# Kernel optimization log

Measured on AMD Instinct MI355X. Metric: run time of the kernel, lower is better.

The kernel has to match this reference:

```python
import jax, jax.numpy as jnp
from jax import lax
import numpy as np

# static config matching init_kwargs
PROPOSAL_COUNT = 1000
NMS_THRESH = 0.7
MIN_SIZE = 16.0
IMG_H, IMG_W = 512, 512
NUM_ANCHORS = 262144
BATCH = 16
PRE_NMS = min(6000, NUM_ANCHORS)


def setup_inputs() -> dict:
    key = jax.random.key(0)
    k1, k2, k3, k4, k5 = jax.random.split(key, 5)
    # realistic anchors: centers uniform in image, sizes in [16, 160]
    cx = jax.random.uniform(k1, (NUM_ANCHORS,), minval=0.0, maxval=float(IMG_W))
    cy = jax.random.uniform(k2, (NUM_ANCHORS,), minval=0.0, maxval=float(IMG_H))
    w = jax.random.uniform(k3, (NUM_ANCHORS,), minval=16.0, maxval=160.0)
    h = jax.random.uniform(k4, (NUM_ANCHORS,), minval=16.0, maxval=160.0)
    anchors = jnp.stack([cx - 0.5 * w, cy - 0.5 * h, cx + 0.5 * w, cy + 0.5 * h], axis=1)
    ka, kb = jax.random.split(k5)
    rpn_class_probs = jax.random.uniform(ka, (BATCH, NUM_ANCHORS, 2), dtype=jnp.float32)
    rpn_bbox_deltas = jax.random.normal(kb, (BATCH, NUM_ANCHORS, 4), dtype=jnp.float32) * 0.2
    return {"anchors": anchors, "rpn_class_probs": rpn_class_probs, "rpn_bbox_deltas": rpn_bbox_deltas}


def apply_box_deltas(anchors, deltas):
    # standard (dx, dy, dw, dh) decode in center form
    w = anchors[:, 2] - anchors[:, 0]
    h = anchors[:, 3] - anchors[:, 1]
    cx = anchors[:, 0] + 0.5 * w
    cy = anchors[:, 1] + 0.5 * h
    cx = cx + deltas[:, 0] * w
    cy = cy + deltas[:, 1] * h
    w = w * jnp.exp(deltas[:, 2])
    h = h * jnp.exp(deltas[:, 3])
    return jnp.stack([cx - 0.5 * w, cy - 0.5 * h, cx + 0.5 * w, cy + 0.5 * h], axis=1)


def nms_keep(boxes, valid):
    # greedy NMS over score-sorted boxes [n,4]; invalid boxes start suppressed
    x1, y1, x2, y2 = boxes[:, 0], boxes[:, 1], boxes[:, 2], boxes[:, 3]
    areas = (x2 - x1) * (y2 - y1)
    n = boxes.shape[0]

    def body(i, state):
        suppressed, keep = state
        is_valid = jnp.logical_not(suppressed[i])
        keep = keep.at[i].set(is_valid)
        xx1 = jnp.maximum(x1[i], x1)
        yy1 = jnp.maximum(y1[i], y1)
        xx2 = jnp.minimum(x2[i], x2)
        yy2 = jnp.minimum(y2[i], y2)
        inter = jnp.maximum(xx2 - xx1, 0.0) * jnp.maximum(yy2 - yy1, 0.0)
        iou = inter / (areas[i] + areas - inter + 1e-9)
        iou = iou.at[i].set(0.0)  # never self-suppress
        suppressed = suppressed | (is_valid & (iou > NMS_THRESH))
        return suppressed, keep

    suppressed0 = jnp.logical_not(valid)
    keep0 = jnp.zeros((n,), dtype=bool)
    _, keep = lax.fori_loop(0, n, body, (suppressed0, keep0))
    return keep


def _per_image(scores, deltas, anchors):
    boxes = apply_box_deltas(anchors, deltas)
    boxes = jnp.stack([
        jnp.clip(boxes[:, 0], 0.0, IMG_W - 1.0),
        jnp.clip(boxes[:, 1], 0.0, IMG_H - 1.0),
        jnp.clip(boxes[:, 2], 0.0, IMG_W - 1.0),
        jnp.clip(boxes[:, 3], 0.0, IMG_H - 1.0),
    ], axis=1)
    ws = boxes[:, 2] - boxes[:, 0]
    hs = boxes[:, 3] - boxes[:, 1]
    valid = (ws >= MIN_SIZE) & (hs >= MIN_SIZE)
    # emulate boolean filter + descending sort with fixed shapes:
    # invalid boxes get -inf score so they sort to the back and start suppressed.
    masked = jnp.where(valid, scores, -jnp.inf)
    order = jnp.argsort(-masked)[:PRE_NMS]
    boxes_s = boxes[order]
    valid_s = valid[order]
    keep = nms_keep(lax.stop_gradient(boxes_s), valid_s)
    idx = jnp.flatnonzero(keep, size=PROPOSAL_COUNT, fill_value=PRE_NMS)
    boxes_pad = jnp.concatenate([boxes_s, jnp.zeros((1, 4), boxes_s.dtype)], axis=0)
    return boxes_pad[idx]  # [proposal_count, 4], zero-padded like torch


def reference(anchors, rpn_class_probs, rpn_bbox_deltas):
    fg_scores = rpn_class_probs[:, :, 1]
    return jax.vmap(_per_image, in_axes=(0, 0, None))(fg_scores, rpn_bbox_deltas, anchors)
```

## Files before the change

kernel.cpp:

```cpp
#include <hip/hip_runtime.h>
#include <cstdint>

#define B 16
#define N 262144
#define PRE 6000
#define KOUT 1000
#define MW 94
#define CW 24
#define NTILE 300
#define ECAP 4096
#define RMAX 64
#define NBIN 2049
#define PREFILT 1967
#define PGATE 0.9599609375f
#define IMGMAX 511.0f
#define NMS_TH 0.7f

typedef unsigned int u32;
typedef unsigned long long u64;

#define OFF_MASK  0ull
#define OFF_SEL   72192000ull
#define OFF_BOX   74289152ull
#define OFF_VAL   75829248ull
#define OFF_HIST  75841536ull
#define OFF_CAB   75972864ull
#define OFF_BCNT  76104192ull
#define OFF_T     76235520ull
#define OFF_M     76235584ull
#define OFF_FLAG  76235648ull
#define OFF_ECNT  76235712ull
#define OFF_EDG   76235776ull
#define OFF_DW    76497920ull
#define OFF_PL    76825600ull
#define OFF_PCNT  78922752ull
#define WS_NEED   78922816ull

__device__ __forceinline__ void box_from(const float4 a, const float4 d,
    float& x1, float& y1, float& x2, float& y2, bool& valid) {
#pragma clang fp contract(off)
  float w  = a.z - a.x;
  float h  = a.w - a.y;
  float cx = a.x + 0.5f * w;
  float cy = a.y + 0.5f * h;
  cx = cx + d.x * w;
  cy = cy + d.y * h;
  w = w * expf(d.z);
  h = h * expf(d.w);
  x1 = cx - 0.5f * w;
  y1 = cy - 0.5f * h;
  x2 = cx + 0.5f * w;
  y2 = cy + 0.5f * h;
  x1 = fminf(fmaxf(x1, 0.0f), IMGMAX);
  y1 = fminf(fmaxf(y1, 0.0f), IMGMAX);
  x2 = fminf(fmaxf(x2, 0.0f), IMGMAX);
  y2 = fminf(fmaxf(y2, 0.0f), IMGMAX);
  valid = ((x2 - x1) >= 16.0f) && ((y2 - y1) >= 16.0f);
}

__device__ __forceinline__ bool iou_gt(float inter, float denom) {
  float d = inter - NMS_TH * denom;
  if (__builtin_expect(fabsf(d) <= 1e-4f * denom, 0))
    return (inter / denom) > NMS_TH;
  return d > 0.0f;
}

__device__ __forceinline__ int bin_of(u32 u) {
  if (u == 0u) return 0;
  float s = __uint_as_float(u & 0x7FFFFFFFu);
  return 1 + min(2047, (int)(s * 2048.0f));
}

__global__ void k_hist(const float4* __restrict__ anch, const float2* __restrict__ probs,
                       const float4* __restrict__ delt, u32* __restrict__ hist,
                       float4* __restrict__ boxes, u64* __restrict__ plist,
                       u32* __restrict__ pcnt) {
  __shared__ u32 sh[128];
  __shared__ u64 pbuf[256];
  __shared__ u32 pcl, pbase;
  int t = threadIdx.x;
  int img = blockIdx.y;
  if (t == 0) pcl = 0;
  if (blockIdx.x == 0 && t < 16)
    boxes[(size_t)img * 6016 + 6000 + t] = make_float4(0.f, 0.f, 0.f, 0.f);
  if (t < 128) sh[t] = 0;
  __syncthreads();
  const float4* pr4 = (const float4*)(probs + (size_t)img * N);
  int b4 = blockIdx.x * 1024 + t;
  float4 p0 = pr4[b4];
  float4 p1 = pr4[b4 + 256];
  float4 p2 = pr4[b4 + 512];
  float4 p3 = pr4[b4 + 768];
  auto handle = [&](float s, int i) {
    if (s >= PGATE) {
      float4 a = anch[i];
      float4 d = delt[(size_t)img * N + i];
      float x1, y1, x2, y2; bool valid;
      box_from(a, d, x1, y1, x2, y2, valid);
      if (valid) {
        int bin = 1 + min(2047, (int)(s * 2048.0f));
        atomicAdd(&sh[bin - 1921], 1u);
        u64 key = ((u64)(__float_as_uint(s) | 0x80000000u) << 32)
                | (u64)(0xFFFFFFFFu - (u32)i);
        u32 p = atomicAdd(&pcl, 1u);
        if (p < 256u) pbuf[p] = key;
      }
    }
  };
  handle(p0.y, 2 * b4);            handle(p0.w, 2 * b4 + 1);
  handle(p1.y, 2 * (b4 + 256));    handle(p1.w, 2 * (b4 + 256) + 1);
  handle(p2.y, 2 * (b4 + 512));    handle(p2.w, 2 * (b4 + 512) + 1);
  handle(p3.y, 2 * (b4 + 768));    handle(p3.w, 2 * (b4 + 768) + 1);
  __syncthreads();
  if (t < 128 && sh[t]) atomicAdd(&hist[img * 2052 + 1921 + t], sh[t]);
  u32 n = min(pcl, 256u);
  if (t == 0) {
    if (pcl > 256u) atomicAdd(&pcnt[img], 1000000u);
    pbase = n ? atomicAdd(&pcnt[img], n) : 0u;
  }
  __syncthreads();
  for (u32 p = t; p < n; p += 256) {
    u32 dp = pbase + p;
    if (dp < 16384u) plist[(size_t)img * 16384 + dp] = pbuf[p];
  }
}

__global__ void k_thresh(const u32* __restrict__ hist, int* __restrict__ Tarr,
                         u32* __restrict__ cab, u32* __restrict__ Marr) {
  int img = blockIdx.x;
  int l = threadIdx.x;
  const u32* hb = hist + img * 2052;
  u32 v0 = hb[1921 + 2 * l];
  u32 v1 = hb[1922 + 2 * l];
  u32 csum = v0 + v1;
  u32 sfx = csum;
  for (int off = 1; off < 64; off <<= 1) {
    u32 tv = __shfl_down(sfx, off);
    if (l + off < 64) sfx += tv;
  }
  u32 excl = sfx - csum;
  u32* cb = cab + img * 2052;
  cb[1921 + 2 * l] = excl + v1;
  cb[1922 + 2 * l] = excl;
  u32 sfxP = __shfl(excl, 22);
  bool ok = (sfxP >= (u32)PRE);
  if (l == 0 && !ok) { Tarr[img] = -1; Marr[img] = 0; }
  if (ok && excl < (u32)PRE && sfx >= (u32)PRE) {
    int T; u32 M;
    if (excl + v1 >= (u32)PRE) { T = 1922 + 2 * l; M = excl + v1; }
    else                       { T = 1921 + 2 * l; M = sfx; }
    Tarr[img] = T; Marr[img] = M;
  }
}

__global__ void k_hist_fb(const float4* __restrict__ anch, const float2* __restrict__ probs,
                          const float4* __restrict__ delt, const int* __restrict__ Tarr,
                          u32* __restrict__ hist) {
  int img = blockIdx.y;
  if (Tarr[img] >= 0) return;
  __shared__ u32 sh[NBIN];
  int t = threadIdx.x;
  for (int p = t; p < NBIN; p += 256) sh[p] = 0;
  __syncthreads();
  int base = blockIdx.x * 1024;
  for (int r = 0; r < 4; r++) {
    int i = base + r * 256 + t;
    float4 a = anch[i];
    float4 d = delt[(size_t)img * N + i];
    float s = probs[(size_t)img * N + i].y;
    float x1, y1, x2, y2; bool valid;
    box_from(a, d, x1, y1, x2, y2, valid);
    int bin = valid ? (1 + min(2047, (int)(s * 2048.0f))) : 0;
    if (bin < PREFILT) atomicAdd(&sh[bin], 1u);
  }
  __syncthreads();
  for (int p = t; p < NBIN; p += 256)
    if (sh[p]) atomicAdd(&hist[img * 2052 + p], sh[p]);
}

__global__ void k_thresh_fb(const u32* __restrict__ hist, int* __restrict__ Tarr,
                            u32* __restrict__ cab, u32* __restrict__ Marr) {
  int img = blockIdx.x;
  if (Tarr[img] >= 0) return;
  int l = threadIdx.x;
  const u32* hb = hist + img * 2052;
  u32 v[32];
  u32 csum = 0;
#pragma unroll
  for (int k = 0; k < 32; k++) { v[k] = hb[l * 32 + 1 + k]; csum += v[k]; }
  u32 sfx = csum;
  for (int off = 1; off < 64; off <<= 1) {
    u32 tv = __shfl_down(sfx, off);
    if (l + off < 64) sfx += tv;
  }
  u32 excl = sfx - csum;
  u32 ss = 0;
  u32 outv[32];
#pragma unroll
  for (int k = 31; k >= 0; k--) { outv[k] = ss + excl; ss += v[k]; }
  u32* cb = cab + img * 2052;
#pragma unroll
  for (int k = 0; k < 32; k++) cb[l * 32 + 1 + k] = outv[k];
  u32 total = __shfl(sfx, 0);
  if (l == 0) cb[0] = total;
  if (l == 0 && total < PRE) { Tarr[img] = 0; Marr[img] = 16384u; }
  if (excl < PRE && sfx >= PRE) {
    u32 acc = excl; int T = 0; u32 Mv = 0;
#pragma unroll
    for (int k = 31; k >= 0; k--) {
      acc += v[k];
      if (acc >= PRE) { T = l * 32 + 1 + k; Mv = acc; break; }
    }
    Tarr[img] = T; Marr[img] = Mv;
  }
}

__global__ void k_compact_fast(const u64* __restrict__ plist, const u32* __restrict__ pcnt,
                               const int* __restrict__ Tarr, const u32* __restrict__ cab,
                               u32* __restrict__ bincnt, u64* __restrict__ sel) {
  int t = threadIdx.x, img = blockIdx.y;
  int T = Tarr[img];
  u32 P = pcnt[img];
  if (T < PREFILT || P > 16384u) return;
  const u32* cb = cab + img * 2052;
  for (u32 i = blockIdx.x * 256u + (u32)t; i < P; i += 8u * 256u) {
    u64 key = plist[(size_t)img * 16384 + i];
    int bin = bin_of((u32)(key >> 32));
    if (bin >= T) {
      u32 p = atomicAdd(&bincnt[img * 2052 + bin], 1u);
      u32 dst = cb[bin] + p;
      if (dst < 16384u) sel[(size_t)img * 16384 + dst] = key;
    }
  }
}

__global__ void k_compact_fb(const float4* __restrict__ anch, const float2* __restrict__ probs,
                             const float4* __restrict__ delt, const u32* __restrict__ pcnt,
                             const int* __restrict__ Tarr, const u32* __restrict__ cab,
                             u32* __restrict__ bincnt, u64* __restrict__ sel) {
  int t = threadIdx.x, img = blockIdx.y;
  int T = Tarr[img];
  u32 P = pcnt[img];
  if (T >= PREFILT && P <= 16384u) return;
  const u32* cb = cab + img * 2052;
  for (int chunk = 0; chunk < 32; chunk++) {
    int i = (blockIdx.x * 32 + chunk) * 256 + t;
    float4 a = anch[i];
    float4 d = delt[(size_t)img * N + i];
    float s = probs[(size_t)img * N + i].y;
    float x1, y1, x2, y2; bool valid;
    box_from(a, d, x1, y1, x2, y2, valid);
    int bin = valid ? (1 + min(2047, (int)(s * 2048.0f))) : 0;
    if (bin >= T) {
      u64 key = ((u64)(valid ? (__float_as_uint(s) | 0x80000000u) : 0u) << 32)
              | (u64)(0xFFFFFFFFu - (u32)i);
      u32 p = atomicAdd(&bincnt[img * 2052 + bin], 1u);
      u32 dst = cb[bin] + p;
      if (dst < 16384u) sel[(size_t)img * 16384 + dst] = key;
    }
  }
}

__global__ void k_rank(const u64* __restrict__ sel, const u32* __restrict__ cab,
                       const u32* __restrict__ hist, const u32* __restrict__ Marr,
                       const float4* __restrict__ anch, const float4* __restrict__ delt,
                       float4* __restrict__ boxes, u64* __restrict__ validw) {
  int t = threadIdx.x, img = blockIdx.y;
  u32 M = min(Marr[img], 16384u);
  u32 ci = blockIdx.x * 256u + (u32)t;
  if (ci >= M) return;
  const u64* sb = sel + (size_t)img * 16384;
  u64 key = sb[ci];
  u32 u = (u32)(key >> 32);
  int bin = bin_of(u);
  const u32* cb = cab + img * 2052;
  u32 segs = cb[bin];
  u32 sege;
  if (bin > 0) sege = cb[bin - 1];
  else         sege = min(16384u, segs + hist[img * 2052 + 0]);
  if (sege > 16384u) sege = 16384u;
  u32 within = 0;
  u32 j = segs;
  for (; j + 4 <= sege; j += 4) {
    within += (sb[j]     > key);
    within += (sb[j + 1] > key);
    within += (sb[j + 2] > key);
    within += (sb[j + 3] > key);
  }
  for (; j < sege; j++) within += (sb[j] > key);
  u32 rank = segs + within;
  if (rank < PRE) {
    u32 gi = 0xFFFFFFFFu - (u32)(key & 0xFFFFFFFFull);
    float4 a = anch[gi];
    float4 d = delt[(size_t)img * N + gi];
    float x1, y1, x2, y2; bool valid;
    box_from(a, d, x1, y1, x2, y2, valid);
    boxes[(size_t)img * 6016 + rank] = make_float4(x1, y1, x2, y2);
    if (u != 0u)
      atomicOr(&validw[img * 96 + (rank >> 6)], 1ull << (rank & 63));
  }
}

__global__ void __launch_bounds__(256) k_mask(
    const float4* __restrict__ boxes, u64* __restrict__ dwbuf,
    u32* __restrict__ ecnt, u32* __restrict__ edges) {
  __shared__ float4 cbox[4][64];
  __shared__ float  carea[4][64];
  __shared__ u32 ebuf[4][128];
  __shared__ u32 ecl[4], ebase[4];
  int t = threadIdx.x;
  int l = t & 63, w = t >> 6;
  int img = blockIdx.y;
  int tid = blockIdx.x * 4 + w;
  float disc = (float)((2 * CW + 1) * (2 * CW + 1) - 8 * tid);
  int rb = (int)(((float)(2 * CW + 1) - sqrtf(disc)) * 0.5f);
  if (rb < 0) rb = 0;
  if (rb > CW - 1) rb = CW - 1;
  while (rb > 0 && (rb * CW - (rb * (rb - 1)) / 2) > tid) rb--;
  while (((rb + 1) * CW - ((rb + 1) * rb) / 2) <= tid) rb++;
  int cb = rb + (tid - (rb * CW - (rb * (rb - 1)) / 2));
  if (l == 0) ecl[w] = 0;
  const float4* bb = boxes + (size_t)img * 6016;
  int r = rb * 64 + l;
  float4 rx = bb[r];
  float ra = (rx.z - rx.x) * (rx.w - rx.y);
  float4 c = bb[cb * 64 + l];
  cbox[w][l] = c;
  carea[w][l] = (c.z - c.x) * (c.w - c.y);
  __syncthreads();
  if (cb == rb) {
    u64 bits = 0ull;
    {
#pragma clang fp contract(off)
#pragma unroll 8
      for (int m = 0; m < 64; m++) {
        float4 cx = cbox[w][m];
        float xx1 = fmaxf(rx.x, cx.x);
        float yy1 = fmaxf(rx.y, cx.y);
        float xx2 = fminf(rx.z, cx.z);
        float yy2 = fminf(rx.w, cx.w);
        float inter = fmaxf(xx2 - xx1, 0.0f) * fmaxf(yy2 - yy1, 0.0f);
        float denom = ra + carea[w][m] - inter + 1e-9f;
        if (iou_gt(inter, denom) && m != l) bits |= (1ull << m);
      }
    }
    dwbuf[((size_t)img * CW + cb) * 64 + l] = bits;
  } else {
    {
#pragma clang fp contract(off)
#pragma unroll 8
      for (int m = 0; m < 64; m++) {
        float4 cx = cbox[w][m];
        float xx1 = fmaxf(rx.x, cx.x);
        float yy1 = fmaxf(rx.y, cx.y);
        float xx2 = fminf(rx.z, cx.z);
        float yy2 = fminf(rx.w, cx.w);
        float inter = fmaxf(xx2 - xx1, 0.0f) * fmaxf(yy2 - yy1, 0.0f);
        float denom = ra + carea[w][m] - inter + 1e-9f;
        if (__builtin_expect(iou_gt(inter, denom), 0)) {
          u32 p = atomicAdd(&ecl[w], 1u);
          if (p < 128u) ebuf[w][p] = (((u32)(cb * 64 + m)) << 16) | (u32)r;
        }
      }
    }
    asm volatile("" ::: "memory");
    u32 n = ecl[w];
    if (n == 0u) return;
    if (n > 128u) n = 128u;
    if (l == 0) {
      if (ecl[w] > 128u) atomicAdd(&ecnt[img], 1000000u);
      ebase[w] = atomicAdd(&ecnt[img], n);
    }
    asm volatile("" ::: "memory");
    u32 eb0 = ebase[w];
    for (u32 p = l; p < n; p += 64) {
      u32 dp = eb0 + p;
      if (dp < ECAP) edges[(size_t)img * ECAP + dp] = ebuf[w][p];
    }
  }
}

__global__ void k_mask_rest(const float4* __restrict__ boxes, u64* __restrict__ mask,
                            const u32* __restrict__ okf) {
  int rb = blockIdx.x, img = blockIdx.y;
  if (okf[img]) return;
  __shared__ float4 cbox[4][64];
  __shared__ float  carea[4][64];
  int t = threadIdx.x;
  int rl = t & 63, g = t >> 6;
  const float4* bb = boxes + (size_t)img * 6016;
  int r = rb * 64 + rl;
  float4 rx = bb[r];
  float ra = (rx.z - rx.x) * (rx.w - rx.y);
  u64* mimg = mask + (size_t)img * 94 * 6000;
  int cb0 = rb;
  int jmax = (94 - cb0 + 3) >> 2;
  for (int j = 0; j < jmax; j++) {
    int cb = cb0 + g + 4 * j;
    bool act = cb < 94;
    __syncthreads();
    if (act) {
      float4 c = bb[cb * 64 + rl];
      cbox[g][rl] = c;
      carea[g][rl] = (c.z - c.x) * (c.w - c.y);
    }
    __syncthreads();
    if (act) {
#pragma clang fp contract(off)
      u64 bits = 0ull;
      for (int m = 0; m < 64; m++) {
        float4 cx = cbox[g][m];
        float xx1 = fmaxf(rx.x, cx.x);
        float yy1 = fmaxf(rx.y, cx.y);
        float xx2 = fminf(rx.z, cx.z);
        float yy2 = fminf(rx.w, cx.w);
        float inter = fmaxf(xx2 - xx1, 0.0f) * fmaxf(yy2 - yy1, 0.0f);
        float denom = ra + carea[g][m] - inter + 1e-9f;
        int c_j = cb * 64 + m;
        if (iou_gt(inter, denom) && c_j != r) bits |= (1ull << m);
      }
      if (r < PRE) mimg[(size_t)cb * 6000 + r] = bits;
    }
  }
}

__global__ void __launch_bounds__(64, 1) k_scan_fast(
    const u64* __restrict__ dwbuf, const u64* __restrict__ validw,
    const float4* __restrict__ boxes, float4* __restrict__ out,
    u32* __restrict__ okf, const u32* __restrict__ ecnt,
    const u32* __restrict__ edges) {
  __shared__ u64 dw[CW * 64];
  __shared__ u64 al[CW], fw[CW], kp[CW], blkX[CW], supX[CW];
  __shared__ u32 eb[ECAP];
  __shared__ unsigned short list[KOUT];
  int l = threadIdx.x;
  int img = blockIdx.x;
  for (int c = 0; c < CW; c++)
    dw[c * 64 + l] = dwbuf[((size_t)img * CW + c) * 64 + l];
  u32 E = ecnt[img];
  if (E > (u32)ECAP) { if (l == 0) okf[img] = 0u; return; }
  for (u32 p = l; p < E; p += 64) eb[p] = edges[(size_t)img * ECAP + p];
  if (l < CW) {
    al[l] = validw[img * 96 + l];
    kp[l] = 0ull; blkX[l] = 0ull; supX[l] = 0ull;
  }
  __syncthreads();
  u64 lmask = (1ull << l) - 1ull;
  bool fail = false;
  for (int round = 0; ; round++) {
    u64 anyv = (l < CW) ? al[l] : 0ull;
#pragma unroll
    for (int off = 32; off >= 1; off >>= 1) anyv |= __shfl_xor(anyv, off);
    if (anyv == 0ull) break;
    if (round >= RMAX) { fail = true; break; }
    for (u32 p = l; p < E; p += 64) {
      u32 e = eb[p];
      u32 tgt = e >> 16, src = e & 0xFFFFu;
      if ((al[src >> 6] >> (src & 63u)) & 1ull)
        atomicOr(&blkX[tgt >> 6], 1ull << (tgt & 63u));
    }
    for (int c = 0; c < CW; c++) {
      u64 a_c = al[c];
      u64 dj = dw[c * 64 + l];
      u64 blkin = __ballot((dj & a_c & lmask) != 0ull);
      if (l == 0) fw[c] = a_c & ~blkin & ~blkX[c];
    }
    for (u32 p = l; p < E; p += 64) {
      u32 e = eb[p];
      u32 tgt = e >> 16, src = e & 0xFFFFu;
      if ((fw[src >> 6] >> (src & 63u)) & 1ull)
        atomicOr(&supX[tgt >> 6], 1ull << (tgt & 63u));
    }
    for (int c = 0; c < CW; c++) {
      u64 f_c = fw[c];
      u64 dj = dw[c * 64 + l];
      u64 supin = __ballot((dj & f_c & lmask) != 0ull);
      if (l == 0) {
        kp[c] |= f_c;
        al[c] = al[c] & ~f_c & ~supin & ~supX[c];
      }
    }
    if (l < CW) { blkX[l] = 0ull; supX[l] = 0ull; }
  }
  u64 kw_l = (!fail && l < CW) ? kp[l] : 0ull;
  u32 pc = (u32)__popcll(kw_l);
  u32 pre = pc;
  for (int off = 1; off < 64; off <<= 1) {
    u32 v2 = __shfl_up(pre, off);
    if (l >= off) pre += v2;
  }
  u32 tot = __shfl(pre, 63);
  bool ok = !fail && (tot >= (u32)KOUT);
  if (l == 0) okf[img] = ok ? 1u : 0u;
  if (!ok) return;
  if (l < CW) {
    u32 b = pre - pc;
    u64 word = kw_l;
    while (word && b < (u32)KOUT) {
      int j = (int)__ffsll(word) - 1;
      word &= word - 1;
      list[b++] = (unsigned short)(l * 64 + j);
    }
  }
  __syncthreads();
  for (int p = l; p < KOUT; p += 64)
    out[(size_t)img * KOUT + p] = boxes[(size_t)img * 6016 + list[p]];
}

__global__ void k_scan_full(const u64* __restrict__ mask, const u64* __restrict__ validw,
                            const float4* __restrict__ boxes, float4* __restrict__ out,
                            const u32* __restrict__ okf) {
  int img = blockIdx.x;
  if (okf[img]) return;
  __shared__ unsigned short kept[KOUT];
  int l = threadIdx.x;
  const u64* vw = validw + img * 96;
  u64 r0 = ~vw[l];
  u64 r1 = (l < MW - 64) ? ~vw[64 + l] : ~0ull;
  const u64* c0p = mask + ((size_t)img * 94 + l) * 6000;
  const u64* c1p = mask + ((size_t)img * 94 + (l < MW - 64 ? 64 + l : 0)) * 6000;

  u64 ca[16], cb[16], na[16], nb2[16];
#pragma unroll
  for (int k = 0; k < 16; k++) {
    ca[k] = c0p[k];
    cb[k] = (l < MW - 64) ? c1p[k] : 0ull;
  }
  int cnt = 0; bool done = false;
  for (int base = 0; base < PRE; base += 16) {
#pragma unroll
    for (int k = 0; k < 16; k++) {
      int rr = base + 16 + k;
      if (rr < PRE) {
        na[k]  = c0p[rr];
        nb2[k] = (l < MW - 64) ? c1p[rr] : 0ull;
      } else { na[k] = 0ull; nb2[k] = 0ull; }
    }
#pragma unroll
    for (int k = 0; k < 16; k++) {
      if (!done) {
        int i = base + k;
        int w = i >> 6;
        u64 wv = (w < 64) ? __shfl(r0, w) : __shfl(r1, w - 64);
        if (!((wv >> (i & 63)) & 1ull)) {
          if (l == 0 && cnt < KOUT) kept[cnt] = (unsigned short)i;
          cnt++;
          r0 |= (l >= w)        ? ca[k] : 0ull;
          r1 |= ((64 + l) >= w) ? cb[k] : 0ull;
          if (cnt >= KOUT) done = true;
        }
      }
    }
    if (done) break;
#pragma unroll
    for (int k = 0; k < 16; k++) { ca[k] = na[k]; cb[k] = nb2[k]; }
  }
  __syncthreads();
  for (int p = l; p < KOUT; p += 64) {
    float4 v = make_float4(0.f, 0.f, 0.f, 0.f);
    if (p < cnt) v = boxes[(size_t)img * 6016 + kept[p]];
    out[(size_t)img * KOUT + p] = v;
  }
}

extern "C" void kernel_launch(void* const* d_in, const int* in_sizes, int n_in,
                              void* d_out, int out_size, void* d_ws, size_t ws_size,
                              hipStream_t stream) {
  const float4* anch  = (const float4*)d_in[0];
  const float2* probs = (const float2*)d_in[1];
  const float4* delt  = (const float4*)d_in[2];
  float4* out = (float4*)d_out;
  char* ws = (char*)d_ws;
  (void)in_sizes; (void)n_in;

  if (ws_size < WS_NEED) {
    (void)hipMemsetAsync(d_out, 0, (size_t)out_size * sizeof(float), stream);
    return;
  }

  u64* mask    = (u64*)(ws + OFF_MASK);
  u64* sel     = (u64*)(ws + OFF_SEL);
  float4* bxs  = (float4*)(ws + OFF_BOX);
  u64* validw  = (u64*)(ws + OFF_VAL);
  u32* hist    = (u32*)(ws + OFF_HIST);
  u32* cab     = (u32*)(ws + OFF_CAB);
  u32* bincnt  = (u32*)(ws + OFF_BCNT);
  int* Tarr    = (int*)(ws + OFF_T);
  u32* Marr    = (u32*)(ws + OFF_M);
  u32* okf     = (u32*)(ws + OFF_FLAG);
  u32* ecnt    = (u32*)(ws + OFF_ECNT);
  u32* edges   = (u32*)(ws + OFF_EDG);
  u64* dwbuf   = (u64*)(ws + OFF_DW);
  u64* plist   = (u64*)(ws + OFF_PL);
  u32* pcnt    = (u32*)(ws + OFF_PCNT);

  (void)hipMemsetAsync(ws + OFF_VAL, 0, 406528, stream);
  (void)hipMemsetAsync(ws + OFF_PCNT, 0, 64, stream);

  dim3 g1h(128, B);
  k_hist<<<g1h, 256, 0, stream>>>(anch, probs, delt, hist, bxs, plist, pcnt);
  k_thresh<<<B, 64, 0, stream>>>(hist, Tarr, cab, Marr);
  dim3 g1(256, B);
  k_hist_fb<<<g1, 256, 0, stream>>>(anch, probs, delt, Tarr, hist);
  k_thresh_fb<<<B, 64, 0, stream>>>(hist, Tarr, cab, Marr);
  dim3 g3(8, B);
  k_compact_fast<<<g3, 256, 0, stream>>>(plist, pcnt, Tarr, cab, bincnt, sel);
  dim3 g3b(32, B);
  k_compact_fb<<<g3b, 256, 0, stream>>>(anch, probs, delt, pcnt, Tarr, cab, bincnt, sel);
  dim3 g4(64, B);
  k_rank<<<g4, 256, 0, stream>>>(sel, cab, hist, Marr, anch, delt, bxs, validw);
  dim3 g5(NTILE / 4, B);
  k_mask<<<g5, 256, 0, stream>>>(bxs, dwbuf, ecnt, edges);
  k_scan_fast<<<B, 64, 0, stream>>>(dwbuf, validw, bxs, out, okf, ecnt, edges);
  dim3 g5b(94, B);
  k_mask_rest<<<g5b, 256, 0, stream>>>(bxs, mask, okf);
  k_scan_full<<<B, 64, 0, stream>>>(mask, validw, bxs, out, okf);
}
```

Measured before the change: 165.8 us.

## Compact gated candidates before box decode and split off-diagonal mask tiles in halves

In k_hist, threads that pass the score gate now only push (score, index) pairs into a shared queue. A second pass spreads box decode and histogram insertion evenly over the block, which removes wave divergence where a few lanes did the expensive decode while the rest idled. In k_mask, each off-diagonal 64x64 tile is split into two 32-column jobs, raising the job count from 300 to 576 to shorten per-wave latency and improve parallelism. This costs an extra barrier and queue overflow handling in k_hist, and duplicated row loads in k_mask.

```diff
diff --git a/kernel.cpp b/kernel.cpp
--- a/kernel.cpp
+++ b/kernel.cpp
@@ -7,7 +7,8 @@
 #define KOUT 1000
 #define MW 94
 #define CW 24
-#define NTILE 300
+#define NOFF 276
+#define NJOB 576
 #define ECAP 4096
 #define RMAX 64
 #define NBIN 2049
@@ -76,11 +77,12 @@
                        float4* __restrict__ boxes, u64* __restrict__ plist,
                        u32* __restrict__ pcnt) {
   __shared__ u32 sh[128];
+  __shared__ u64 qbuf[192];
   __shared__ u64 pbuf[256];
-  __shared__ u32 pcl, pbase;
+  __shared__ u32 qcl, pcl, pbase;
   int t = threadIdx.x;
   int img = blockIdx.y;
-  if (t == 0) pcl = 0;
+  if (t == 0) { qcl = 0; pcl = 0; }
   if (blockIdx.x == 0 && t < 16)
     boxes[(size_t)img * 6016 + 6000 + t] = make_float4(0.f, 0.f, 0.f, 0.f);
   if (t < 128) sh[t] = 0;
@@ -91,31 +93,42 @@
   float4 p1 = pr4[b4 + 256];
   float4 p2 = pr4[b4 + 512];
   float4 p3 = pr4[b4 + 768];
-  auto handle = [&](float s, int i) {
+  auto check = [&](float s, int i) {
     if (s >= PGATE) {
-      float4 a = anch[i];
-      float4 d = delt[(size_t)img * N + i];
-      float x1, y1, x2, y2; bool valid;
-      box_from(a, d, x1, y1, x2, y2, valid);
-      if (valid) {
-        int bin = 1 + min(2047, (int)(s * 2048.0f));
-        atomicAdd(&sh[bin - 1921], 1u);
-        u64 key = ((u64)(__float_as_uint(s) | 0x80000000u) << 32)
-                | (u64)(0xFFFFFFFFu - (u32)i);
-        u32 p = atomicAdd(&pcl, 1u);
-        if (p < 256u) pbuf[p] = key;
-      }
+      u32 q = atomicAdd(&qcl, 1u);
+      if (q < 192u)
+        qbuf[q] = ((u64)__float_as_uint(s) << 32) | (u64)(u32)i;
     }
   };
-  handle(p0.y, 2 * b4);            handle(p0.w, 2 * b4 + 1);
-  handle(p1.y, 2 * (b4 + 256));    handle(p1.w, 2 * (b4 + 256) + 1);
-  handle(p2.y, 2 * (b4 + 512));    handle(p2.w, 2 * (b4 + 512) + 1);
-  handle(p3.y, 2 * (b4 + 768));    handle(p3.w, 2 * (b4 + 768) + 1);
+  check(p0.y, 2 * b4);            check(p0.w, 2 * b4 + 1);
+  check(p1.y, 2 * (b4 + 256));    check(p1.w, 2 * (b4 + 256) + 1);
+  check(p2.y, 2 * (b4 + 512));    check(p2.w, 2 * (b4 + 512) + 1);
+  check(p3.y, 2 * (b4 + 768));    check(p3.w, 2 * (b4 + 768) + 1);
+  __syncthreads();
+  u32 qn = min(qcl, 192u);
+  for (u32 q = t; q < qn; q += 256) {
+    u64 qv = qbuf[q];
+    float s = __uint_as_float((u32)(qv >> 32));
+    int i = (int)(u32)qv;
+    float4 a = anch[i];
+    float4 d = delt[(size_t)img * N + i];
+    float x1, y1, x2, y2; bool valid;
+    box_from(a, d, x1, y1, x2, y2, valid);
+    if (valid) {
+      int bin = 1 + min(2047, (int)(s * 2048.0f));
+      atomicAdd(&sh[bin - 1921], 1u);
+      u64 key = ((u64)(__float_as_uint(s) | 0x80000000u) << 32)
+              | (u64)(0xFFFFFFFFu - (u32)i);
+      u32 p = atomicAdd(&pcl, 1u);
+      if (p < 256u) pbuf[p] = key;
+    }
+  }
   __syncthreads();
   if (t < 128 && sh[t]) atomicAdd(&hist[img * 2052 + 1921 + t], sh[t]);
   u32 n = min(pcl, 256u);
   if (t == 0) {
-    if (pcl > 256u) atomicAdd(&pcnt[img], 1000000u);
+    if (qcl > 192u || pcl > 256u)
+      atomicAdd(&pcnt[img], 1000000u);
     pbase = n ? atomicAdd(&pcnt[img], n) : 0u;
   }
   __syncthreads();
@@ -311,24 +324,36 @@
   int t = threadIdx.x;
   int l = t & 63, w = t >> 6;
   int img = blockIdx.y;
-  int tid = blockIdx.x * 4 + w;
-  float disc = (float)((2 * CW + 1) * (2 * CW + 1) - 8 * tid);
-  int rb = (int)(((float)(2 * CW + 1) - sqrtf(disc)) * 0.5f);
-  if (rb < 0) rb = 0;
-  if (rb > CW - 1) rb = CW - 1;
-  while (rb > 0 && (rb * CW - (rb * (rb - 1)) / 2) > tid) rb--;
-  while (((rb + 1) * CW - ((rb + 1) * rb) / 2) <= tid) rb++;
-  int cb = rb + (tid - (rb * CW - (rb * (rb - 1)) / 2));
+  int jid = blockIdx.x * 4 + w;
+  bool diag = (jid < CW);
+  int rb, cb, half = 0, nc;
+  if (diag) { rb = cb = jid; nc = 64; }
+  else {
+    int k = jid - CW;
+    int oid = k >> 1;
+    half = k & 1;
+    int r0 = (int)((47.0f - sqrtf((float)(47 * 47 - 8 * oid))) * 0.5f);
+    if (r0 < 0) r0 = 0;
+    if (r0 > CW - 2) r0 = CW - 2;
+    while (r0 > 0 && ((r0 * (47 - r0)) >> 1) > oid) r0--;
+    while ((((r0 + 1) * (46 - r0)) >> 1) <= oid) r0++;
+    rb = r0;
+    cb = rb + 1 + (oid - ((rb * (47 - rb)) >> 1));
+    nc = 32;
+  }
   if (l == 0) ecl[w] = 0;
   const float4* bb = boxes + (size_t)img * 6016;
   int r = rb * 64 + l;
   float4 rx = bb[r];
   float ra = (rx.z - rx.x) * (rx.w - rx.y);
-  float4 c = bb[cb * 64 + l];
-  cbox[w][l] = c;
-  carea[w][l] = (c.z - c.x) * (c.w - c.y);
-  __syncthreads();
-  if (cb == rb) {
+  int colbase = cb * 64 + half * 32;
+  if (l < nc) {
+    float4 c = bb[colbase + l];
+    cbox[w][l] = c;
+    carea[w][l] = (c.z - c.x) * (c.w - c.y);
+  }
+  __syncthreads();
+  if (diag) {
     u64 bits = 0ull;
     {
 #pragma clang fp contract(off)
@@ -349,7 +374,7 @@
     {
 #pragma clang fp contract(off)
 #pragma unroll 8
-      for (int m = 0; m < 64; m++) {
+      for (int m = 0; m < 32; m++) {
         float4 cx = cbox[w][m];
         float xx1 = fmaxf(rx.x, cx.x);
         float yy1 = fmaxf(rx.y, cx.y);
@@ -359,7 +384,7 @@
         float denom = ra + carea[w][m] - inter + 1e-9f;
         if (__builtin_expect(iou_gt(inter, denom), 0)) {
           u32 p = atomicAdd(&ecl[w], 1u);
-          if (p < 128u) ebuf[w][p] = (((u32)(cb * 64 + m)) << 16) | (u32)r;
+          if (p < 128u) ebuf[w][p] = (((u32)(colbase + m)) << 16) | (u32)r;
         }
       }
     }
@@ -609,7 +634,7 @@
   k_compact_fb<<<g3b, 256, 0, stream>>>(anch, probs, delt, pcnt, Tarr, cab, bincnt, sel);
   dim3 g4(64, B);
   k_rank<<<g4, 256, 0, stream>>>(sel, cab, hist, Marr, anch, delt, bxs, validw);
-  dim3 g5(NTILE / 4, B);
+  dim3 g5(NJOB / 4, B);
   k_mask<<<g5, 256, 0, stream>>>(bxs, dwbuf, ecnt, edges);
   k_scan_fast<<<B, 64, 0, stream>>>(dwbuf, validw, bxs, out, okf, ecnt, edges);
   dim3 g5b(94, B);
```

Result: no change. 167.8 us (+1.2%).
